# Kernel tuning notes

Measured on AMD Instinct MI355X. Metric: run time of the kernel, lower is better.

Reference implementation:

```python
import jax, jax.numpy as jnp
import numpy as np
from jax import lax

DEPTH, DIM, HEADS, DHEAD = 4, 384, 8, 64
INNER = HEADS * DHEAD          # 512
HID = int(DIM * 0.25)          # 96 (hardcoded in Transformer_Conv)
B, Hg, Wg = 8, 32, 32
N = Hg * Wg
SCALE = DHEAD ** -0.5
EPS = 1e-5


def _layer_norm(x, w, b):
    mu = jnp.mean(x, axis=-1, keepdims=True)
    var = jnp.mean(jnp.square(x - mu), axis=-1, keepdims=True)
    return (x - mu) * lax.rsqrt(var + EPS) * w + b


def setup_inputs() -> dict:
    key = jax.random.key(0)
    ks = jax.random.split(key, 8)
    s = 0.02
    return {
        "x": jax.random.normal(ks[0], (B, N, DIM), jnp.float32),
        "ln1_w": jnp.ones((DEPTH, DIM), jnp.float32),
        "ln1_b": jnp.zeros((DEPTH, DIM), jnp.float32),
        "w_qkv": jax.random.normal(ks[1], (DEPTH, DIM, 3 * INNER), jnp.float32) * s,
        "w_out": jax.random.normal(ks[2], (DEPTH, INNER, DIM), jnp.float32) * s,
        "b_out": jnp.zeros((DEPTH, DIM), jnp.float32),
        "ln2_w": jnp.ones((DEPTH, DIM), jnp.float32),
        "ln2_b": jnp.zeros((DEPTH, DIM), jnp.float32),
        "fc1_w": jax.random.normal(ks[3], (DEPTH, DIM, HID), jnp.float32) * s,
        "fc1_b": jnp.zeros((DEPTH, HID), jnp.float32),
        "dw_w": jax.random.normal(ks[4], (DEPTH, HID, 1, 3, 3), jnp.float32) * s,
        "dw_b": jnp.zeros((DEPTH, HID), jnp.float32),
        "fc2_w": jax.random.normal(ks[5], (DEPTH, HID, DIM), jnp.float32) * s,
        "fc2_b": jnp.zeros((DEPTH, DIM), jnp.float32),
        "H": Hg,
        "W": Wg,
    }


def _forward(x, ln1_w, ln1_b, w_qkv, w_out, b_out, ln2_w, ln2_b,
             fc1_w, fc1_b, dw_w, dw_b, fc2_w, fc2_b, H, W):
    b, n, c = x.shape
    attn_last = None
    for l in range(DEPTH):
        # ---- PreNorm + Attention (with post-softmax cross-layer residual) ----
        xn = _layer_norm(x, ln1_w[l], ln1_b[l])
        qkv = xn @ w_qkv[l]                                   # [b, n, 3*inner]
        q, k, v = jnp.split(qkv, 3, axis=-1)
        q = q.reshape(b, n, HEADS, DHEAD).transpose(0, 2, 1, 3)  # bhnd
        k = k.reshape(b, n, HEADS, DHEAD).transpose(0, 2, 1, 3)
        v = v.reshape(b, n, HEADS, DHEAD).transpose(0, 2, 1, 3)
        dots = jnp.einsum("bhid,bhjd->bhij", q, k) * SCALE
        attn = jax.nn.softmax(dots, axis=-1)
        if attn_last is not None:
            attn = attn + attn_last
        attn_last = attn
        out = jnp.einsum("bhij,bhjd->bhid", attn, v)
        out = out.transpose(0, 2, 1, 3).reshape(b, n, INNER)
        x = out @ w_out[l] + b_out[l] + x
        # ---- ConvFFN: LN -> fc1 -> depthwise conv 3x3 -> GELU -> fc2 ----
        y = _layer_norm(x, ln2_w[l], ln2_b[l])
        y = y @ fc1_w[l] + fc1_b[l]                            # [b, n, HID]
        y4 = y.transpose(0, 2, 1).reshape(b, HID, H, W)
        y4 = lax.conv_general_dilated(
            y4, dw_w[l], window_strides=(1, 1), padding="SAME",
            feature_group_count=HID,
            dimension_numbers=("NCHW", "OIHW", "NCHW"),
        ) + dw_b[l][None, :, None, None]
        y = y4.reshape(b, HID, n).transpose(0, 2, 1)
        y = jax.nn.gelu(y, approximate=False)                  # torch nn.GELU (erf)
        x = y @ fc2_w[l] + fc2_b[l] + x
    return x


def reference(x, ln1_w, ln1_b, w_qkv, w_out, b_out, ln2_w, ln2_b,
              fc1_w, fc1_b, dw_w, dw_b, fc2_w, fc2_b, H, W):
    return _forward(x, ln1_w, ln1_b, w_qkv, w_out, b_out, ln2_w, ln2_b,
                    fc1_w, fc1_b, dw_w, dw_b, fc2_w, fc2_b, H, W)
```

## Files before the change

### kernel.cpp

```cpp
#include <hip/hip_runtime.h>
#include <hip/hip_bf16.h>
#include <math.h>

#define DEPTH 4
#define DIM 384
#define HEADS 8
#define DHEAD 64
#define INNER 512
#define HID 96
#define BATCH 8
#define NTOK 1024
#define ROWS (BATCH*NTOK)

typedef __attribute__((ext_vector_type(8))) _Float16 half8;
typedef __attribute__((ext_vector_type(4))) _Float16 half4;
typedef __attribute__((ext_vector_type(4))) float f32x4;


__global__ __launch_bounds__(256) void ln_kernel(const float* __restrict__ x,
                                                 const float* __restrict__ w,
                                                 const float* __restrict__ b,
                                                 _Float16* __restrict__ outF) {
  const int row = blockIdx.x * 4 + (threadIdx.x >> 6);
  const int lane = threadIdx.x & 63;
  const float* xr = x + (size_t)row * DIM;
  float v[6];
  float s = 0.f;
#pragma unroll
  for (int i = 0; i < 6; ++i) {
    v[i] = xr[lane + i * 64];
    s += v[i];
  }
#pragma unroll
  for (int m = 1; m < 64; m <<= 1) s += __shfl_xor(s, m);
  const float mean = s * (1.0f / DIM);
  float sq = 0.f;
#pragma unroll
  for (int i = 0; i < 6; ++i) {
    v[i] -= mean;
    sq += v[i] * v[i];
  }
#pragma unroll
  for (int m = 1; m < 64; m <<= 1) sq += __shfl_xor(sq, m);
  const float rs = rsqrtf(sq * (1.0f / DIM) + 1e-5f);
  const int f = row >> 4, lr = row & 15;
#pragma unroll
  for (int i = 0; i < 6; ++i) {
    const int k = lane + i * 64;
    outF[(((size_t)f * 12 + (k >> 5)) * 16 + lr) * 32 + (k & 31)] =
        (_Float16)(v[i] * rs * w[k] + b[k]);
  }
}

__global__ __launch_bounds__(256) void transposeW(const float* __restrict__ in0,
                                                  _Float16* __restrict__ out0,
                                                  int K, int N, int Npad) {
  __shared__ float t[32][33];
  const int l = blockIdx.z;
  const int KS = K >> 5;
  const float* in = in0 + (size_t)l * K * N;
  _Float16* out = out0 + (size_t)l * Npad * K;
  const int k0 = blockIdx.x * 32, n0 = blockIdx.y * 32;
  const int tx = threadIdx.x & 31, ty = threadIdx.x >> 5;
#pragma unroll
  for (int i = 0; i < 4; ++i) {
    int k = k0 + ty + i * 8, n = n0 + tx;
    t[ty + i * 8][tx] = (n < N) ? in[(size_t)k * N + n] : 0.f;
  }
  __syncthreads();
  const int k = k0 + tx;
#pragma unroll
  for (int i = 0; i < 4; ++i) {
    int n = n0 + ty + i * 8;
    if (n < Npad)
      out[(((size_t)(n >> 4) * KS + (k >> 5)) * 16 + (n & 15)) * 32 + (k & 31)] =
          (_Float16)t[tx][ty + i * 8];
  }
}

template <bool BIAS, bool RES, bool OUT16, int KT, int NT>
__global__ __launch_bounds__(256) void hgemm(const _Float16* __restrict__ AF,
                                             const _Float16* __restrict__ BF,
                                             const float* __restrict__ bias,
                                             const float* __restrict__ res,
                                             void* __restrict__ Cout) {
  constexpr int KS = KT / 32;
  const int tid = threadIdx.x;
  const int wave = tid >> 6, lane = tid & 63;
  const int wm = wave >> 1, wn = wave & 1;
  const int g = lane >> 4, lr = lane & 15;
  const int m0 = blockIdx.x * 128 + wm * 64;
  const int n0 = blockIdx.y * 128 + wn * 64;
  const int fA = m0 >> 4, fB = n0 >> 4;
  const int lo = lr * 32 + g * 8;
  f32x4 acc[4][4];
#pragma unroll
  for (int i = 0; i < 4; ++i)
#pragma unroll
    for (int j = 0; j < 4; ++j) acc[i][j] = {0.f, 0.f, 0.f, 0.f};

  for (int ks = 0; ks < KS; ++ks) {
    half8 af[4], bf[4];
#pragma unroll
    for (int i = 0; i < 4; ++i)
      af[i] = *(const half8*)(AF + ((size_t)(fA + i) * KS + ks) * 512 + lo);
#pragma unroll
    for (int j = 0; j < 4; ++j)
      bf[j] = *(const half8*)(BF + ((size_t)(fB + j) * KS + ks) * 512 + lo);
#pragma unroll
    for (int i = 0; i < 4; ++i)
#pragma unroll
      for (int j = 0; j < 4; ++j)
        acc[i][j] =
            __builtin_amdgcn_mfma_f32_16x16x32_f16(af[i], bf[j], acc[i][j], 0, 0, 0);
  }

#pragma unroll
  for (int i = 0; i < 4; ++i) {
#pragma unroll
    for (int j = 0; j < 4; ++j) {
      const int n = n0 + j * 16 + lr;
      if (NT % 128 == 0 || n < NT) {
        float bb = BIAS ? bias[n] : 0.f;
#pragma unroll
        for (int jj = 0; jj < 4; ++jj) {
          const int m = m0 + i * 16 + g * 4 + jj;
          float v = acc[i][j][jj] + bb;
          const size_t idx = (size_t)m * NT + n;
          if (RES) v += res[idx];
          if (OUT16)
            ((_Float16*)Cout)[idx] = (_Float16)v;
          else
            ((float*)Cout)[idx] = v;
        }
      }
    }
  }
}

__global__ __launch_bounds__(256) void hgemm_fc1(const _Float16* __restrict__ AF,
                                                 const _Float16* __restrict__ BF,
                                                 const float* __restrict__ bias,
                                                 _Float16* __restrict__ C) {
  const int tid = threadIdx.x;
  const int wave = tid >> 6, lane = tid & 63;
  const int g = lane >> 4, lr = lane & 15;
  const int m0 = blockIdx.x * 32;
  const int fA = m0 >> 4, fB = wave * 2;
  const int lo = lr * 32 + g * 8;
  f32x4 acc[2][2];
#pragma unroll
  for (int i = 0; i < 2; ++i)
#pragma unroll
    for (int j = 0; j < 2; ++j) acc[i][j] = {0.f, 0.f, 0.f, 0.f};

  for (int ks = 0; ks < 12; ++ks) {
    half8 af[2], bf[2];
#pragma unroll
    for (int i = 0; i < 2; ++i)
      af[i] = *(const half8*)(AF + ((size_t)(fA + i) * 12 + ks) * 512 + lo);
#pragma unroll
    for (int j = 0; j < 2; ++j)
      bf[j] = *(const half8*)(BF + ((size_t)(fB + j) * 12 + ks) * 512 + lo);
#pragma unroll
    for (int i = 0; i < 2; ++i)
#pragma unroll
      for (int j = 0; j < 2; ++j)
        acc[i][j] =
            __builtin_amdgcn_mfma_f32_16x16x32_f16(af[i], bf[j], acc[i][j], 0, 0, 0);
  }

#pragma unroll
  for (int i = 0; i < 2; ++i)
#pragma unroll
    for (int j = 0; j < 2; ++j) {
      const int n = wave * 32 + j * 16 + lr;
      if (n < HID) {
        const float bb = bias[n];
#pragma unroll
        for (int jj = 0; jj < 4; ++jj) {
          const int m = m0 + i * 16 + g * 4 + jj;
          C[(size_t)m * HID + n] = (_Float16)(acc[i][j][jj] + bb);
        }
      }
    }
}

__global__ __launch_bounds__(256) void hgemm_qkv(const _Float16* __restrict__ AF,
                                                 const _Float16* __restrict__ BF,
                                                 _Float16* __restrict__ qF,
                                                 _Float16* __restrict__ kT,
                                                 _Float16* __restrict__ vTn) {
  const int tid = threadIdx.x;
  const int wave = tid >> 6, lane = tid & 63;
  const int wm = wave >> 1, wn = wave & 1;
  const int g = lane >> 4, lr = lane & 15;
  const int m0 = blockIdx.x * 128 + wm * 64;
  const int n0 = blockIdx.y * 128 + wn * 64;
  const int fA = m0 >> 4, fB = n0 >> 4;
  const int lo = lr * 32 + g * 8;
  f32x4 acc[4][4];
#pragma unroll
  for (int i = 0; i < 4; ++i)
#pragma unroll
    for (int j = 0; j < 4; ++j) acc[i][j] = {0.f, 0.f, 0.f, 0.f};

  for (int ks = 0; ks < 12; ++ks) {
    half8 af[4], bf[4];
#pragma unroll
    for (int i = 0; i < 4; ++i)
      af[i] = *(const half8*)(AF + ((size_t)(fA + i) * 12 + ks) * 512 + lo);
#pragma unroll
    for (int j = 0; j < 4; ++j)
      bf[j] = *(const half8*)(BF + ((size_t)(fB + j) * 12 + ks) * 512 + lo);
#pragma unroll
    for (int i = 0; i < 4; ++i)
#pragma unroll
      for (int j = 0; j < 4; ++j)
        acc[i][j] =
            __builtin_amdgcn_mfma_f32_16x16x32_f16(af[i], bf[j], acc[i][j], 0, 0, 0);
  }

  if (n0 < 512) {
#pragma unroll
    for (int i = 0; i < 4; ++i)
#pragma unroll
      for (int j = 0; j < 4; ++j) {
        const int n = n0 + j * 16 + lr;
#pragma unroll
        for (int jj = 0; jj < 4; ++jj) {
          const int m = m0 + i * 16 + g * 4 + jj;
          qF[(((size_t)(m >> 4) * 16 + (n >> 5)) * 16 + (m & 15)) * 32 + (n & 31)] =
              (_Float16)acc[i][j][jj];
        }
      }
  } else if (n0 < 1024) {
#pragma unroll
    for (int j = 0; j < 4; ++j) {
      const int n = n0 + j * 16 + lr;
      const int hk = (n - 512) >> 6, d = (n - 512) & 63;
      const int sb = d >> 5, dd = d & 31;
#pragma unroll
      for (int i = 0; i < 4; ++i)
#pragma unroll
        for (int jj = 0; jj < 4; ++jj) {
          const int m = m0 + i * 16 + g * 4 + jj;
          const int bb = m >> 10, tok = m & 1023;
          const int f = tok >> 4, tr = tok & 15;
          kT[((((size_t)(bb * 8 + hk) * 64 + f) * 2 + sb) * 16 + tr) * 32 + dd] =
              (_Float16)acc[i][j][jj];
        }
    }
  } else {
    const int bb = m0 >> 10;
    const int tok0 = (m0 & 1023) + g * 4;
#pragma unroll
    for (int j = 0; j < 4; ++j) {
      const int dg = n0 + j * 16 + lr - 1024;
      const int hk = dg >> 6, d = dg & 63;
#pragma unroll
      for (int i = 0; i < 4; ++i) {
        const int tok = tok0 + i * 16;
        const int kb = tok >> 5, tk = tok & 31;
        half4 t = {(_Float16)acc[i][j][0], (_Float16)acc[i][j][1],
                   (_Float16)acc[i][j][2], (_Float16)acc[i][j][3]};
        *(half4*)(vTn + (((size_t)(bb * 8 + hk) * 32 + kb) * 64 + d) * 32 + tk) = t;
      }
    }
  }
}

__device__ __forceinline__ int pidx(int r, int c) {
  return ((((r << 11) + (c << 1)) ^ ((r & 15) << 4)) >> 1);
}

__global__ __launch_bounds__(512) void attn_kernel(
    const _Float16* __restrict__ qF, const _Float16* __restrict__ kT,
    const _Float16* __restrict__ vTn, _Float16* __restrict__ store,
    _Float16* __restrict__ aoutF, int has_prev, int write_store) {
  __shared__ __align__(16) char smem[32768];
  _Float16* P = (_Float16*)smem;
  float (*red)[16][68] = (float (*)[16][68])smem;
  __shared__ float partial[8][16];
  __shared__ float invs[16];

  const int tid = threadIdx.x;
  const int wave = tid >> 6, lane = tid & 63;
  const int g = lane >> 4, lr = lane & 15;
  const int blk = blockIdx.x;
  const int xcd = blk & 7, j0 = blk >> 3;
  const int bh = xcd * 8 + (j0 >> 6), rt = j0 & 63;
  const int b = bh >> 3, h = bh & 7;
  const int r0 = rt << 4;
  const int fq = (b * NTOK + r0) >> 4;

  const _Float16* kbase = kT + (size_t)bh * 64 * 1024;
  const _Float16* vbase = vTn + (size_t)bh * 32 * 2048;
  const size_t gbase = ((size_t)bh * NTOK + r0) * 1024;

  half8 prev[4];
  if (has_prev) {
#pragma unroll
    for (int it = 0; it < 4; ++it) {
      const int e = tid + it * 512;
      const int r = e >> 7, c8 = (e & 127) << 3;
      prev[it] = *(const half8*)(store + gbase + ((size_t)r << 10) + c8);
    }
  }

  const half8 a0 =
      *(const half8*)(qF + (((size_t)fq * 16 + h * 2) * 16 + lr) * 32 + g * 8);
  const half8 a1 = *(const half8*)(
      qF + (((size_t)fq * 16 + h * 2 + 1) * 16 + lr) * 32 + g * 8);

  float p[8][4];
  float rs[4] = {0.f, 0.f, 0.f, 0.f};
  __builtin_amdgcn_s_setprio(1);
#pragma unroll
  for (int fl = 0; fl < 8; ++fl) {
    const int f = wave * 8 + fl;
    const _Float16* kb = kbase + (size_t)f * 1024 + lr * 32 + g * 8;
    half8 b0 = *(const half8*)(kb);
    half8 b1 = *(const half8*)(kb + 512);
    f32x4 acc = {0.f, 0.f, 0.f, 0.f};
    acc = __builtin_amdgcn_mfma_f32_16x16x32_f16(a0, b0, acc, 0, 0, 0);
    acc = __builtin_amdgcn_mfma_f32_16x16x32_f16(a1, b1, acc, 0, 0, 0);
#pragma unroll
    for (int j = 0; j < 4; ++j) {
      float e = __expf(acc[j] * 0.125f);
      p[fl][j] = e;
      rs[j] += e;
    }
  }
  __builtin_amdgcn_s_setprio(0);
#pragma unroll
  for (int j = 0; j < 4; ++j) {
    rs[j] += __shfl_xor(rs[j], 1);
    rs[j] += __shfl_xor(rs[j], 2);
    rs[j] += __shfl_xor(rs[j], 4);
    rs[j] += __shfl_xor(rs[j], 8);
  }
  if (lr == 0) {
#pragma unroll
    for (int j = 0; j < 4; ++j) partial[wave][g * 4 + j] = rs[j];
  }
  __syncthreads();
  if (tid < 16) {
    float s = 0.f;
#pragma unroll
    for (int w = 0; w < 8; ++w) s += partial[w][tid];
    invs[tid] = 1.0f / s;
  }
  __syncthreads();

#pragma unroll
  for (int fl = 0; fl < 8; ++fl) {
    const int c = wave * 128 + fl * 16 + lr;
#pragma unroll
    for (int j = 0; j < 4; ++j) {
      const int r = g * 4 + j;
      P[pidx(r, c)] = (_Float16)(p[fl][j] * invs[r]);
    }
  }
  __syncthreads();

  half8 pvreg[4];
#pragma unroll
  for (int it = 0; it < 4; ++it) {
    const int e = tid + it * 512;
    const int r = e >> 7, c8 = (e & 127) << 3;
    half8 pv = *(half8*)(P + pidx(r, c8));
    if (has_prev) {
#pragma unroll
      for (int k = 0; k < 8; ++k)
        pv[k] = (_Float16)((float)pv[k] + (float)prev[it][k]);
      *(half8*)(P + pidx(r, c8)) = pv;
    }
    pvreg[it] = pv;
  }
  __syncthreads();

  const int nf = wave & 3, kh = wave >> 2;
  f32x4 oacc = {0.f, 0.f, 0.f, 0.f};
  __builtin_amdgcn_s_setprio(1);
#pragma unroll
  for (int ks = 0; ks < 16; ++ks) {
    const int kb = kh * 16 + ks;
    half8 af = *(half8*)(P + pidx(lr, kb * 32 + g * 8));
    half8 bfv = *(const half8*)(vbase + ((size_t)kb * 64 + nf * 16 + lr) * 32 + g * 8);
    oacc = __builtin_amdgcn_mfma_f32_16x16x32_f16(af, bfv, oacc, 0, 0, 0);
  }
  __builtin_amdgcn_s_setprio(0);
  __syncthreads();

  if (write_store) {
#pragma unroll
    for (int it = 0; it < 4; ++it) {
      const int e = tid + it * 512;
      const int r = e >> 7, c8 = (e & 127) << 3;
      *(half8*)(store + gbase + ((size_t)r << 10) + c8) = pvreg[it];
    }
  }

#pragma unroll
  for (int j = 0; j < 4; ++j) red[kh][g * 4 + j][nf * 16 + lr] = oacc[j];
  __syncthreads();
#pragma unroll
  for (int it = 0; it < 2; ++it) {
    const int e = tid + it * 512;
    const int r = e >> 6, d = e & 63;
    float s = red[0][r][d] + red[1][r][d];
    aoutF[(((size_t)fq * 16 + h * 2 + (d >> 5)) * 16 + r) * 32 + (d & 31)] =
        (_Float16)s;
  }
}

__global__ __launch_bounds__(256) void dwconv_gelu(const _Float16* __restrict__ y,
                                                   const float* __restrict__ w,
                                                   const float* __restrict__ bs,
                                                   _Float16* __restrict__ outF) {
  const int blk = blockIdx.x;
  const int bb = blk / 96;
  const int rem = blk - bb * 96;
  const int hh = rem / 3, cg = rem - (rem / 3) * 3;
#pragma unroll
  for (int it = 0; it < 4; ++it) {
    const int e = threadIdx.x + it * 256;
    const int c = cg * 32 + (e & 31), ww = e >> 5;
    float acc = bs[c];
#pragma unroll
    for (int dh = 0; dh < 3; ++dh) {
      int ih = hh + dh - 1;
      if (ih < 0 || ih >= 32) continue;
#pragma unroll
      for (int dw = 0; dw < 3; ++dw) {
        int iw = ww + dw - 1;
        if (iw < 0 || iw >= 32) continue;
        acc += (float)y[((size_t)(bb * NTOK + ih * 32 + iw)) * HID + c] *
               w[c * 9 + dh * 3 + dw];
      }
    }
    float gl = 0.5f * acc * (1.f + erff(acc * 0.70710678118f));
    const int f = bb * 64 + hh * 2 + (ww >> 4);
    outF[(((size_t)f * 3 + cg) * 16 + (ww & 15)) * 32 + (e & 31)] = (_Float16)gl;
  }
}

extern "C" void kernel_launch(void* const* d_in, const int* in_sizes, int n_in,
                              void* d_out, int out_size, void* d_ws,
                              size_t ws_size, hipStream_t stream) {
  const float* x_in  = (const float*)d_in[0];
  const float* ln1_w = (const float*)d_in[1];
  const float* ln1_b = (const float*)d_in[2];
  const float* w_qkv = (const float*)d_in[3];
  const float* w_out = (const float*)d_in[4];
  const float* b_out = (const float*)d_in[5];
  const float* ln2_w = (const float*)d_in[6];
  const float* ln2_b = (const float*)d_in[7];
  const float* fc1_w = (const float*)d_in[8];
  const float* fc1_b = (const float*)d_in[9];
  const float* dw_w  = (const float*)d_in[10];
  const float* dw_b  = (const float*)d_in[11];
  const float* fc2_w = (const float*)d_in[12];
  const float* fc2_b = (const float*)d_in[13];

  float* x = (float*)d_out;

  char* ws = (char*)d_ws;
  _Float16* xnF   = (_Float16*)ws; ws += (size_t)ROWS * DIM * 2;
  _Float16* qF    = (_Float16*)ws; ws += (size_t)ROWS * 512 * 2;
  _Float16* kT    = (_Float16*)ws; ws += (size_t)64 * 64 * 1024 * 2;
  _Float16* vTn   = (_Float16*)ws; ws += (size_t)64 * 32 * 2048 * 2;
  _Float16* aoutF = (_Float16*)ws; ws += (size_t)ROWS * INNER * 2;
  _Float16* y1    = (_Float16*)ws; ws += (size_t)ROWS * HID * 2;
  _Float16* y2F   = (_Float16*)ws; ws += (size_t)ROWS * HID * 2;
  _Float16* wqkvT = (_Float16*)ws; ws += (size_t)DEPTH * 1536 * DIM * 2;
  _Float16* woutT = (_Float16*)ws; ws += (size_t)DEPTH * DIM * INNER * 2;
  _Float16* fc1T  = (_Float16*)ws; ws += (size_t)DEPTH * 128 * DIM * 2;
  _Float16* fc2T  = (_Float16*)ws; ws += (size_t)DEPTH * DIM * HID * 2;
  _Float16* astore = (_Float16*)ws;

  transposeW<<<dim3(12, 48, DEPTH), 256, 0, stream>>>(w_qkv, wqkvT, DIM,
                                                      1536, 1536);
  transposeW<<<dim3(16, 12, DEPTH), 256, 0, stream>>>(w_out, woutT, INNER,
                                                      DIM, DIM);
  transposeW<<<dim3(12, 4, DEPTH), 256, 0, stream>>>(fc1_w, fc1T, DIM, HID,
                                                     128);
  transposeW<<<dim3(3, 12, DEPTH), 256, 0, stream>>>(fc2_w, fc2T, HID, DIM,
                                                     DIM);

  hipMemcpyAsync(x, x_in, (size_t)ROWS * DIM * 4, hipMemcpyDeviceToDevice,
                 stream);

  for (int l = 0; l < DEPTH; ++l) {
    ln_kernel<<<ROWS / 4, 256, 0, stream>>>(x, ln1_w + l * DIM,
                                            ln1_b + l * DIM, xnF);
    hgemm_qkv<<<dim3(64, 12), 256, 0, stream>>>(
        xnF, wqkvT + (size_t)l * 1536 * DIM, qF, kT, vTn);
    attn_kernel<<<4096, 512, 0, stream>>>(qF, kT, vTn, astore, aoutF,
                                          l > 0 ? 1 : 0,
                                          l < DEPTH - 1 ? 1 : 0);
    hgemm<true, true, false, INNER, DIM><<<dim3(64, 3), 256, 0, stream>>>(
        aoutF, woutT + (size_t)l * DIM * INNER, b_out + l * DIM, x, x);
    ln_kernel<<<ROWS / 4, 256, 0, stream>>>(x, ln2_w + l * DIM,
                                            ln2_b + l * DIM, xnF);
    hgemm_fc1<<<ROWS / 32, 256, 0, stream>>>(
        xnF, fc1T + (size_t)l * 128 * DIM, fc1_b + l * HID, y1);
    dwconv_gelu<<<768, 256, 0, stream>>>(y1, dw_w + l * HID * 9,
                                         dw_b + l * HID, y2F);
    hgemm<true, true, false, HID, DIM><<<dim3(64, 3), 256, 0, stream>>>(
        y2F, fc2T + (size_t)l * DIM * HID, fc2_b + l * DIM, x, x);
  }
}
```

Baseline: 650.4 us.

## Fuse LayerNorm into out-proj and fc2 GEMM epilogues with full-row tiles

The generic 128x128-tile GEMM for the attention out-projection and fc2 is replaced by a kernel where each block computes a full 32-row by 384-column output tile. The block stages the result plus bias and residual in shared memory, writes x back, and computes the next LayerNorm (ln2 or the next layer's ln1) in the epilogue, emitting the fragment-layout fp16 input for the following GEMM. This removes seven standalone LN launches and their extra read of x. The cost is smaller M tiles with more B-operand reloads per block, plus a large shared-memory buffer that may limit occupancy.

```diff
diff --git a/kernel.cpp b/kernel.cpp
--- a/kernel.cpp
+++ b/kernel.cpp
@@ -78,61 +78,90 @@
   }
 }
 
-template <bool BIAS, bool RES, bool OUT16, int KT, int NT>
-__global__ __launch_bounds__(256) void hgemm(const _Float16* __restrict__ AF,
-                                             const _Float16* __restrict__ BF,
-                                             const float* __restrict__ bias,
-                                             const float* __restrict__ res,
-                                             void* __restrict__ Cout) {
-  constexpr int KS = KT / 32;
+template <int KS, bool DO_LN>
+__global__ __launch_bounds__(256) void gemm_ln(const _Float16* __restrict__ AF,
+                                               const _Float16* __restrict__ BF,
+                                               const float* __restrict__ bias,
+                                               float* __restrict__ x,
+                                               const float* __restrict__ lnw,
+                                               const float* __restrict__ lnb,
+                                               _Float16* __restrict__ outF) {
+  __shared__ float C[32][388];
   const int tid = threadIdx.x;
   const int wave = tid >> 6, lane = tid & 63;
-  const int wm = wave >> 1, wn = wave & 1;
   const int g = lane >> 4, lr = lane & 15;
-  const int m0 = blockIdx.x * 128 + wm * 64;
-  const int n0 = blockIdx.y * 128 + wn * 64;
-  const int fA = m0 >> 4, fB = n0 >> 4;
+  const int m0 = blockIdx.x * 32;
+  const int fA = m0 >> 4;
   const int lo = lr * 32 + g * 8;
-  f32x4 acc[4][4];
-#pragma unroll
-  for (int i = 0; i < 4; ++i)
-#pragma unroll
-    for (int j = 0; j < 4; ++j) acc[i][j] = {0.f, 0.f, 0.f, 0.f};
+  f32x4 acc[2][6];
+#pragma unroll
+  for (int i = 0; i < 2; ++i)
+#pragma unroll
+    for (int j = 0; j < 6; ++j) acc[i][j] = {0.f, 0.f, 0.f, 0.f};
 
   for (int ks = 0; ks < KS; ++ks) {
-    half8 af[4], bf[4];
-#pragma unroll
-    for (int i = 0; i < 4; ++i)
+    half8 af[2], bf[6];
+#pragma unroll
+    for (int i = 0; i < 2; ++i)
       af[i] = *(const half8*)(AF + ((size_t)(fA + i) * KS + ks) * 512 + lo);
 #pragma unroll
-    for (int j = 0; j < 4; ++j)
-      bf[j] = *(const half8*)(BF + ((size_t)(fB + j) * KS + ks) * 512 + lo);
-#pragma unroll
-    for (int i = 0; i < 4; ++i)
-#pragma unroll
-      for (int j = 0; j < 4; ++j)
+    for (int j = 0; j < 6; ++j)
+      bf[j] = *(const half8*)(BF + ((size_t)(wave * 6 + j) * KS + ks) * 512 + lo);
+#pragma unroll
+    for (int i = 0; i < 2; ++i)
+#pragma unroll
+      for (int j = 0; j < 6; ++j)
         acc[i][j] =
             __builtin_amdgcn_mfma_f32_16x16x32_f16(af[i], bf[j], acc[i][j], 0, 0, 0);
   }
 
 #pragma unroll
-  for (int i = 0; i < 4; ++i) {
-#pragma unroll
-    for (int j = 0; j < 4; ++j) {
-      const int n = n0 + j * 16 + lr;
-      if (NT % 128 == 0 || n < NT) {
-        float bb = BIAS ? bias[n] : 0.f;
-#pragma unroll
-        for (int jj = 0; jj < 4; ++jj) {
-          const int m = m0 + i * 16 + g * 4 + jj;
-          float v = acc[i][j][jj] + bb;
-          const size_t idx = (size_t)m * NT + n;
-          if (RES) v += res[idx];
-          if (OUT16)
-            ((_Float16*)Cout)[idx] = (_Float16)v;
-          else
-            ((float*)Cout)[idx] = v;
-        }
+  for (int i = 0; i < 2; ++i)
+#pragma unroll
+    for (int j = 0; j < 6; ++j) {
+      const int n = wave * 96 + j * 16 + lr;
+      const float bb = bias[n];
+#pragma unroll
+      for (int jj = 0; jj < 4; ++jj) {
+        const int r = i * 16 + g * 4 + jj;
+        C[r][n] = acc[i][j][jj] + bb + x[(size_t)(m0 + r) * DIM + n];
+      }
+    }
+  __syncthreads();
+
+#pragma unroll
+  for (int it = 0; it < 8; ++it) {
+    const int r = it * 4 + wave;
+    float v[6];
+    float s = 0.f;
+#pragma unroll
+    for (int i = 0; i < 6; ++i) {
+      v[i] = C[r][lane + i * 64];
+      s += v[i];
+    }
+#pragma unroll
+    for (int i = 0; i < 6; ++i)
+      x[(size_t)(m0 + r) * DIM + lane + i * 64] = v[i];
+    if (DO_LN) {
+#pragma unroll
+      for (int m = 1; m < 64; m <<= 1) s += __shfl_xor(s, m);
+      const float mean = s * (1.0f / DIM);
+      float sq = 0.f;
+#pragma unroll
+      for (int i = 0; i < 6; ++i) {
+        v[i] -= mean;
+        sq += v[i] * v[i];
+      }
+#pragma unroll
+      for (int m = 1; m < 64; m <<= 1) sq += __shfl_xor(sq, m);
+      const float rs = rsqrtf(sq * (1.0f / DIM) + 1e-5f);
+      const int row = m0 + r;
+      const int f = row >> 4, flr = row & 15;
+#pragma unroll
+      for (int i = 0; i < 6; ++i) {
+        const int k = lane + i * 64;
+        outF[(((size_t)f * 12 + (k >> 5)) * 16 + flr) * 32 + (k & 31)] =
+            (_Float16)(v[i] * rs * lnw[k] + lnb[k]);
       }
     }
   }
@@ -492,23 +521,29 @@
   hipMemcpyAsync(x, x_in, (size_t)ROWS * DIM * 4, hipMemcpyDeviceToDevice,
                  stream);
 
+  ln_kernel<<<ROWS / 4, 256, 0, stream>>>(x, ln1_w, ln1_b, xnF);
+
   for (int l = 0; l < DEPTH; ++l) {
-    ln_kernel<<<ROWS / 4, 256, 0, stream>>>(x, ln1_w + l * DIM,
-                                            ln1_b + l * DIM, xnF);
     hgemm_qkv<<<dim3(64, 12), 256, 0, stream>>>(
         xnF, wqkvT + (size_t)l * 1536 * DIM, qF, kT, vTn);
     attn_kernel<<<4096, 512, 0, stream>>>(qF, kT, vTn, astore, aoutF,
                                           l > 0 ? 1 : 0,
                                           l < DEPTH - 1 ? 1 : 0);
-    hgemm<true, true, false, INNER, DIM><<<dim3(64, 3), 256, 0, stream>>>(
-        aoutF, woutT + (size_t)l * DIM * INNER, b_out + l * DIM, x, x);
-    ln_kernel<<<ROWS / 4, 256, 0, stream>>>(x, ln2_w + l * DIM,
-                                            ln2_b + l * DIM, xnF);
+    gemm_ln<16, true><<<ROWS / 32, 256, 0, stream>>>(
+        aoutF, woutT + (size_t)l * DIM * INNER, b_out + l * DIM, x,
+        ln2_w + l * DIM, ln2_b + l * DIM, xnF);
     hgemm_fc1<<<ROWS / 32, 256, 0, stream>>>(
         xnF, fc1T + (size_t)l * 128 * DIM, fc1_b + l * HID, y1);
     dwconv_gelu<<<768, 256, 0, stream>>>(y1, dw_w + l * HID * 9,
                                          dw_b + l * HID, y2F);
-    hgemm<true, true, false, HID, DIM><<<dim3(64, 3), 256, 0, stream>>>(
-        y2F, fc2T + (size_t)l * DIM * HID, fc2_b + l * DIM, x, x);
-  }
-}
+    if (l < DEPTH - 1) {
+      gemm_ln<3, true><<<ROWS / 32, 256, 0, stream>>>(
+          y2F, fc2T + (size_t)l * DIM * HID, fc2_b + l * DIM, x,
+          ln1_w + (l + 1) * DIM, ln1_b + (l + 1) * DIM, xnF);
+    } else {
+      gemm_ln<3, false><<<ROWS / 32, 256, 0, stream>>>(
+          y2F, fc2T + (size_t)l * DIM * HID, fc2_b + l * DIM, x, nullptr,
+          nullptr, nullptr);
+    }
+  }
+}
```

After: 664.7 us. 2.2% more time.

## Store cross-layer attention in MFMA fragment layout and drop softmax barriers

Applied to the files above, without the earlier changes.

The persistent attention-probability buffer that carries the cross-layer residual is now stored in the MFMA accumulator fragment order. Each lane therefore reads its previous-layer values and writes its new ones directly from registers, instead of round-tripping through shared memory. Each thread also computes the row-sum reciprocals itself from the partial sums, which removes one block barrier and a separate shared-memory pass that added the previous attention. The cost is narrower half4 global accesses, and the layout of the store buffer changes, which is consistent only because this kernel is the sole producer and consumer of it.

```diff
diff --git a/kernel.cpp b/kernel.cpp
--- a/kernel.cpp
+++ b/kernel.cpp
@@ -281,8 +281,7 @@
   __shared__ __align__(16) char smem[32768];
   _Float16* P = (_Float16*)smem;
   float (*red)[16][68] = (float (*)[16][68])smem;
-  __shared__ float partial[8][16];
-  __shared__ float invs[16];
+  __shared__ __align__(16) float partial[8][16];
 
   const int tid = threadIdx.x;
   const int wave = tid >> 6, lane = tid & 63;
@@ -296,16 +295,15 @@
 
   const _Float16* kbase = kT + (size_t)bh * 64 * 1024;
   const _Float16* vbase = vTn + (size_t)bh * 32 * 2048;
-  const size_t gbase = ((size_t)bh * NTOK + r0) * 1024;
-
-  half8 prev[4];
+  const size_t gbase = ((size_t)bh * 64 + rt) * 16384;
+  const int fragoff = lr * 16 + g * 4;
+
+  half4 prev4[8];
   if (has_prev) {
 #pragma unroll
-    for (int it = 0; it < 4; ++it) {
-      const int e = tid + it * 512;
-      const int r = e >> 7, c8 = (e & 127) << 3;
-      prev[it] = *(const half8*)(store + gbase + ((size_t)r << 10) + c8);
-    }
+    for (int fl = 0; fl < 8; ++fl)
+      prev4[fl] = *(const half4*)(store + gbase +
+                                  (size_t)(wave * 8 + fl) * 256 + fragoff);
   }
 
   const half8 a0 =
@@ -345,38 +343,29 @@
     for (int j = 0; j < 4; ++j) partial[wave][g * 4 + j] = rs[j];
   }
   __syncthreads();
-  if (tid < 16) {
-    float s = 0.f;
-#pragma unroll
-    for (int w = 0; w < 8; ++w) s += partial[w][tid];
-    invs[tid] = 1.0f / s;
-  }
-  __syncthreads();
-
+
+  f32x4 sv = {0.f, 0.f, 0.f, 0.f};
+#pragma unroll
+  for (int w = 0; w < 8; ++w) {
+    const float4 pw = *(const float4*)&partial[w][g * 4];
+    sv[0] += pw.x; sv[1] += pw.y; sv[2] += pw.z; sv[3] += pw.w;
+  }
+  float inv[4];
+#pragma unroll
+  for (int j = 0; j < 4; ++j) inv[j] = 1.0f / sv[j];
+
+  half4 t4[8];
 #pragma unroll
   for (int fl = 0; fl < 8; ++fl) {
     const int c = wave * 128 + fl * 16 + lr;
 #pragma unroll
     for (int j = 0; j < 4; ++j) {
-      const int r = g * 4 + j;
-      P[pidx(r, c)] = (_Float16)(p[fl][j] * invs[r]);
-    }
-  }
-  __syncthreads();
-
-  half8 pvreg[4];
-#pragma unroll
-  for (int it = 0; it < 4; ++it) {
-    const int e = tid + it * 512;
-    const int r = e >> 7, c8 = (e & 127) << 3;
-    half8 pv = *(half8*)(P + pidx(r, c8));
-    if (has_prev) {
-#pragma unroll
-      for (int k = 0; k < 8; ++k)
-        pv[k] = (_Float16)((float)pv[k] + (float)prev[it][k]);
-      *(half8*)(P + pidx(r, c8)) = pv;
-    }
-    pvreg[it] = pv;
+      float val = p[fl][j] * inv[j];
+      if (has_prev) val += (float)prev4[fl][j];
+      const _Float16 hv = (_Float16)val;
+      t4[fl][j] = hv;
+      P[pidx(g * 4 + j, c)] = hv;
+    }
   }
   __syncthreads();
 
@@ -395,11 +384,9 @@
 
   if (write_store) {
 #pragma unroll
-    for (int it = 0; it < 4; ++it) {
-      const int e = tid + it * 512;
-      const int r = e >> 7, c8 = (e & 127) << 3;
-      *(half8*)(store + gbase + ((size_t)r << 10) + c8) = pvreg[it];
-    }
+    for (int fl = 0; fl < 8; ++fl)
+      *(half4*)(store + gbase + (size_t)(wave * 8 + fl) * 256 + fragoff) =
+          t4[fl];
   }
 
 #pragma unroll
```

Measured after the change: 652.9 us. Within noise of the previous version (+0.4%).
